# Kernel optimization log

Measured on AMD Instinct MI355X. Metric: run time of the kernel, lower is better.

## Reference

```python
import jax, jax.numpy as jnp
import numpy as np

D_MODEL = 1024
SEL_DIM = 64
CONFIGS = [(4, 32), (8, 64), (16, 128)]  # (heads, dim)
B, T = 2, 2048


def setup_inputs() -> dict:
    key = jax.random.key(0)
    ks = jax.random.split(key, 20)
    s = 0.02  # init scale for stability
    inp = {
        "x": jax.random.normal(ks[0], (B, T, D_MODEL), jnp.float32),
        "sel_w1": jax.random.normal(ks[1], (SEL_DIM, D_MODEL), jnp.float32) * s,
        "sel_b1": jnp.zeros((SEL_DIM,), jnp.float32),
        "sel_w2": jax.random.normal(ks[2], (SEL_DIM, SEL_DIM), jnp.float32) * s,
        "sel_b2": jnp.zeros((SEL_DIM,), jnp.float32),
        "sel_w3": jax.random.normal(ks[3], (len(CONFIGS), SEL_DIM), jnp.float32) * s,
        "sel_b3": jnp.zeros((len(CONFIGS),), jnp.float32),
    }
    for i, (h, d) in enumerate(CONFIGS):
        inp[f"qw{i}"] = jax.random.normal(ks[4 + 3 * i], (h * d, D_MODEL), jnp.float32) * s
        inp[f"kw{i}"] = jax.random.normal(ks[5 + 3 * i], (d, D_MODEL), jnp.float32) * s
        inp[f"ww{i}"] = jax.random.normal(ks[6 + 3 * i], (h, D_MODEL), jnp.float32) * s
    return inp


def _seq_features(x):
    # x: [b,t,d]
    b, t, d = x.shape
    seq_mean = jnp.mean(x, axis=1, keepdims=True)            # [b,1,d]
    seq_std = jnp.std(x, axis=1, keepdims=True, ddof=1)      # torch.std is unbiased
    pos = (jnp.arange(t, dtype=x.dtype) / t)[None, :, None]  # [1,t,1] broadcast to [b,t,d]
    return x + seq_mean + seq_std + pos * 0.1


def _forward(x, sel_w1, sel_b1, sel_w2, sel_b2, sel_w3, sel_b3,
             qw0, kw0, ww0, qw1, kw1, ww1, qw2, kw2, ww2):
    b, t, dm = x.shape
    feats = _seq_features(x)
    h1 = jax.nn.relu(feats @ sel_w1.T + sel_b1)
    h2 = jax.nn.relu(h1 @ sel_w2.T + sel_b2)
    config_probs = jax.nn.softmax(h2 @ sel_w3.T + sel_b3, axis=-1)  # [b,t,ncfg]

    per_cfg = [(qw0, kw0, ww0), (qw1, kw1, ww1), (qw2, kw2, ww2)]
    final = jnp.zeros((b, t, t), dtype=x.dtype)
    for i, ((heads, dim), (qw, kw, ww)) in enumerate(zip(CONFIGS, per_cfg)):
        q = (x @ qw.T).reshape(b, t, heads, dim)   # [b,t,h,d]
        k = x @ kw.T                               # [b,s,d]
        w = x @ ww.T                               # [b,t,h]
        dots = jnp.einsum('bthd,bsd->bths', q, k)  # [b,t,h,s]
        score = jnp.einsum('bths,bth->bts', jax.nn.relu(dots), w)  # relu*weight, sum heads
        final = final + config_probs[:, :, i:i + 1] * score
    return final


def reference(x, sel_w1, sel_b1, sel_w2, sel_b2, sel_w3, sel_b3,
              qw0, kw0, ww0, qw1, kw1, ww1, qw2, kw2, ww2):
    return _forward(x, sel_w1, sel_b1, sel_w2, sel_b2, sel_w3, sel_b3,
                    qw0, kw0, ww0, qw1, kw1, ww1, qw2, kw2, ww2)
```

## Files before the change

### kernel.cpp

```cpp
#include <hip/hip_runtime.h>
#include <hip/hip_fp16.h>
#include <cstdint>
#include <cstddef>
#include <math.h>

#define B_ 2
#define T_ 2048
#define D_ 1024
#define M_ (B_*T_)

#define QO0 0
#define KO0 128
#define WO0 160
#define QO1 168
#define KO1 680
#define WO1 744
#define QO2 752
#define KO2 2800
#define WO2 2928
#define SELO 2944
#define LDN 3072

typedef float f32x16 __attribute__((ext_vector_type(16)));
typedef short bf16x8 __attribute__((ext_vector_type(8)));
typedef unsigned short u16;

__device__ __forceinline__ u16 f2bf(float f) {
    unsigned int u = __float_as_uint(f);
    unsigned int r = (u + 0x7fffu + ((u >> 16) & 1u)) >> 16;
    return (u16)r;
}
__device__ __forceinline__ float bf2f(u16 b) {
    return __uint_as_float(((unsigned int)b) << 16);
}

__device__ __forceinline__ void gload16(const void* g, void* l) {
    __builtin_amdgcn_global_load_lds(
        (const __attribute__((address_space(1))) unsigned int*)g,
        (__attribute__((address_space(3))) unsigned int*)l,
        16, 0, 0);
}

__device__ __forceinline__ void stage_plane(const u16* src_base, int row_stride, int k0,
                                            int rg, int lane, u16* dst) {
    int rl  = lane >> 2;
    int row = rg * 16 + rl;
    int q   = (lane & 3) ^ (rl & 3) ^ ((rl >> 2) & 3);
    const u16* s = src_base + (size_t)row * row_stride + k0 + q * 8;
    gload16(s, dst + rg * 512);
}

__global__ void stats1(const float* __restrict__ x, float* __restrict__ part,
                       float* __restrict__ part2, u16* __restrict__ Xh) {
    int d  = blockIdx.x * 256 + threadIdx.x;
    int tc = blockIdx.y;
    int b  = blockIdx.z;
    size_t base = (size_t)b * T_ * D_ + (size_t)tc * 128 * D_ + d;
    float s = 0.f, s2 = 0.f;
    for (int t = 0; t < 128; ++t) {
        float v = x[base + (size_t)t * D_];
        s += v; s2 += v * v;
        Xh[base + (size_t)t * D_] = f2bf(v);
    }
    part [(b * 16 + tc) * D_ + d] = s;
    part2[(b * 16 + tc) * D_ + d] = s2;
}

__global__ void stats2(const float* __restrict__ part, const float* __restrict__ part2,
                       const float* __restrict__ w1,
                       float* __restrict__ msd, float* __restrict__ s1) {
    __shared__ float msL[1024];
    __shared__ float ps[64][17];
    __shared__ float pw[64][17];
    int b = blockIdx.x, tid = threadIdx.x;
    float s = 0.f, s2 = 0.f;
    for (int i = 0; i < 16; ++i) {
        s  += part [(b * 16 + i) * D_ + tid];
        s2 += part2[(b * 16 + i) * D_ + tid];
    }
    float mean = s / (float)T_;
    float var  = (s2 - (float)T_ * mean * mean) / (float)(T_ - 1);
    msL[tid] = mean + sqrtf(fmaxf(var, 0.f));
    __syncthreads();
    int j = tid >> 4, cc = tid & 15;
    float am = 0.f, aw = 0.f;
    const float* wr = w1 + (size_t)j * D_ + cc * 64;
    const float* mr = msL + cc * 64;
    for (int dd = 0; dd < 64; ++dd) { float w = wr[dd]; am += mr[dd] * w; aw += w; }
    ps[j][cc] = am; pw[j][cc] = aw;
    __syncthreads();
    if (tid < 64) {
        float sm = 0.f, sw = 0.f;
        for (int i = 0; i < 16; ++i) { sm += ps[tid][i]; sw += pw[tid][i]; }
        msd[b * 64 + tid] = sm;
        if (b == 0) s1[tid] = sw;
    }
}

__global__ void split_w(const float* __restrict__ qw0, const float* __restrict__ kw0,
                        const float* __restrict__ ww0, const float* __restrict__ qw1,
                        const float* __restrict__ kw1, const float* __restrict__ ww1,
                        const float* __restrict__ qw2, const float* __restrict__ kw2,
                        const float* __restrict__ ww2, const float* __restrict__ w1s,
                        u16* __restrict__ Wh) {
    int row = blockIdx.x;
    int col = threadIdx.x * 4;
    const float* src = nullptr;
    if      (row < 128)  src = qw0 + (size_t)row * D_;
    else if (row < 160)  src = kw0 + (size_t)(row - 128) * D_;
    else if (row < 164)  src = ww0 + (size_t)(row - 160) * D_;
    else if (row < 168)  src = nullptr;
    else if (row < 680)  src = qw1 + (size_t)(row - 168) * D_;
    else if (row < 744)  src = kw1 + (size_t)(row - 680) * D_;
    else if (row < 752)  src = ww1 + (size_t)(row - 744) * D_;
    else if (row < 2800) src = qw2 + (size_t)(row - 752) * D_;
    else if (row < 2928) src = kw2 + (size_t)(row - 2800) * D_;
    else if (row < 2944) src = ww2 + (size_t)(row - 2928) * D_;
    else if (row < 3008) src = w1s + (size_t)(row - 2944) * D_;
    float4 v = src ? *(const float4*)(src + col) : make_float4(0.f, 0.f, 0.f, 0.f);
    ushort4 h;
    h.x = f2bf(v.x); h.y = f2bf(v.y); h.z = f2bf(v.z); h.w = f2bf(v.w);
    *(ushort4*)&Wh[(size_t)row * D_ + col] = h;
}

__global__ __launch_bounds__(256, 4) void proj_gemm(
    const u16* __restrict__ Xh, const u16* __restrict__ Wh, u16* __restrict__ Ph) {
    __shared__ u16 As[2][4096], Bs[2][4096];
    int tid = threadIdx.x;
    int wave = tid >> 6, lane = tid & 63;
    int bm = blockIdx.x * 128, bn = blockIdx.y * 128;
    int wt = wave >> 1, wn = wave & 1;
    int fm = lane & 31, hv = lane >> 5;
    int tkey = (fm & 3) ^ ((fm >> 2) & 3);
    f32x16 acc[2][2];
#pragma unroll
    for (int i = 0; i < 2; ++i)
#pragma unroll
        for (int j = 0; j < 2; ++j)
#pragma unroll
            for (int r = 0; r < 16; ++r) acc[i][j][r] = 0.f;

    const u16* xh = Xh + (size_t)bm * D_;
    const u16* wh = Wh + (size_t)bn * D_;

    auto stage = [&](int buf, int k0) {
#pragma unroll
        for (int i = 0; i < 4; ++i) {
            int j = wave * 4 + i;
            int pl = j >> 3, rg = j & 7;
            stage_plane(pl ? wh : xh, D_, k0, rg, lane, pl ? Bs[buf] : As[buf]);
        }
    };

    stage(0, 0);
    for (int kc = 0; kc < 32; ++kc) {
        __syncthreads();
        if (kc + 1 < 32) stage((kc + 1) & 1, (kc + 1) * 32);
        const u16* ah = As[kc & 1];
        const u16* bh = Bs[kc & 1];
#pragma unroll
        for (int ks = 0; ks < 2; ++ks) {
            int slot8 = ((ks * 2 + hv) ^ tkey) * 8;
            bf16x8 a_h[2], b_h[2];
#pragma unroll
            for (int t = 0; t < 2; ++t) {
                a_h[t] = *(const bf16x8*)&ah[(wt * 64 + t * 32 + fm) * 32 + slot8];
                b_h[t] = *(const bf16x8*)&bh[(wn * 64 + t * 32 + fm) * 32 + slot8];
            }
#pragma unroll
            for (int ti = 0; ti < 2; ++ti)
#pragma unroll
                for (int tj = 0; tj < 2; ++tj)
                    acc[ti][tj] = __builtin_amdgcn_mfma_f32_32x32x16_bf16(a_h[ti], b_h[tj], acc[ti][tj], 0, 0, 0);
        }
    }
#pragma unroll
    for (int ti = 0; ti < 2; ++ti)
#pragma unroll
        for (int tj = 0; tj < 2; ++tj)
#pragma unroll
            for (int r = 0; r < 16; ++r) {
                int row = bm + wt * 64 + ti * 32 + (r & 3) + 8 * (r >> 2) + 4 * (lane >> 5);
                int col = bn + wn * 64 + tj * 32 + (lane & 31);
                Ph[(size_t)row * LDN + col] = f2bf(acc[ti][tj][r]);
            }
}

__global__ void selector2(const u16* __restrict__ Ph,
                          const float* __restrict__ msd, const float* __restrict__ s1,
                          const float* __restrict__ b1, const float* __restrict__ w2,
                          const float* __restrict__ b2, const float* __restrict__ w3,
                          const float* __restrict__ b3, __half* __restrict__ WP) {
    __shared__ float h1s[4][64];
    __shared__ float h2s[4][64];
    __shared__ float lg[4][3];
    int tid = threadIdx.x;
    int slot = tid >> 6, j = tid & 63;
    int bt = blockIdx.x * 4 + slot;
    int b = bt >> 11, t = bt & 2047;
    size_t pidx = (size_t)bt * LDN + SELO + j;
    float v = bf2f(Ph[pidx])
            + msd[b * 64 + j] + 0.1f * ((float)t / (float)T_) * s1[j] + b1[j];
    h1s[slot][j] = fmaxf(v, 0.f);
    __syncthreads();
    float a2 = b2[j];
#pragma unroll 8
    for (int d = 0; d < 64; ++d) a2 = fmaf(h1s[slot][d], w2[j * 64 + d], a2);
    h2s[slot][j] = fmaxf(a2, 0.f);
    __syncthreads();
    if (j < 3) {
        float a3 = b3[j];
        for (int d = 0; d < 64; ++d) a3 = fmaf(h2s[slot][d], w3[j * 64 + d], a3);
        lg[slot][j] = a3;
    }
    __syncthreads();
    if (j < 28) {
        float m = fmaxf(lg[slot][0], fmaxf(lg[slot][1], lg[slot][2]));
        float e0 = expf(lg[slot][0] - m), e1 = expf(lg[slot][1] - m), e2 = expf(lg[slot][2] - m);
        float inv = 1.f / (e0 + e1 + e2);
        int wcol = (j < 4) ? (WO0 + j) : ((j < 12) ? (WO1 + j - 4) : (WO2 + j - 12));
        float p = ((j < 4) ? e0 : ((j < 12) ? e1 : e2)) * inv;
        float w = bf2f(Ph[(size_t)bt * LDN + wcol]);
        WP[(size_t)(b * 28 + j) * T_ + t] = __float2half(w * p);
    }
}

__global__ __launch_bounds__(256, 4) void score_kernel(
    const u16* __restrict__ Ph, const __half* __restrict__ WP, float* __restrict__ out) {
    __shared__ u16 Qs[2][4096];
    __shared__ u16 Ks[4][2048];
    __shared__ __half wpL[3584];
    int tid = threadIdx.x;
    int wave = tid >> 6, lane = tid & 63;
    int wt = wave >> 1, wn = wave & 1;
    int fm = lane & 31, hv = lane >> 5;
    int tkey = (fm & 3) ^ ((fm >> 2) & 3);

    int n = blockIdx.x;
    int qt = (n & 7) * 4 + (n >> 8);
    int b = qt >> 4, t0 = (qt & 15) * 128;
    int s0 = ((n >> 3) & 31) * 64;

    const u16* Pq = Ph + (size_t)(b * T_ + t0) * LDN;
    const u16* Pk = Ph + (size_t)(b * T_ + s0) * LDN;

    auto stageQ = [&](int buf, int qcol) {
#pragma unroll
        for (int i = 0; i < 2; ++i) {
            int rg = wave * 2 + i;
            stage_plane(Pq, LDN, qcol, rg, lane, Qs[buf]);
        }
    };

#pragma unroll
    for (int i = 0; i < 3; ++i) {
        int j = i * 4 + wave;
        int pl = j >> 2, rg = j & 3;
        int col = (pl == 0) ? KO0 : ((pl == 1) ? KO1 : KO1 + 32);
        stage_plane(Pk, LDN, col, rg, lane, Ks[pl]);
    }
#pragma unroll
    for (int i = 0; i < 2; ++i) {
        int j = i * 4 + wave;
        if (j < 7) {
            const __half* src = WP + (size_t)(b * 28 + j * 4 + (lane >> 4)) * T_ + t0 + (lane & 15) * 8;
            gload16(src, (u16*)wpL + j * 512);
        }
    }
    stageQ(0, QO0);

    f32x16 outacc[2], dots[2];
#pragma unroll
    for (int i = 0; i < 2; ++i)
#pragma unroll
        for (int r = 0; r < 16; ++r) { outacc[i][r] = 0.f; dots[i][r] = 0.f; }

    for (int c = 0; c < 84; ++c) {
        int kp, g;
        if (c < 4)       { kp = 0; g = c; }
        else if (c < 20) { int u = c - 4;  kp = 1 + (u & 1); g = (u & 1) ? (4 + (u >> 1)) : -1; }
        else             { int u = c - 20; kp = u & 3; g = ((u & 3) == 3) ? (12 + (u >> 2)) : -1; }

        __syncthreads();
        if (c < 83) {
            int nc = c + 1;
            int nq = (nc < 4) ? (QO0 + nc * 32)
                   : ((nc < 20) ? (QO1 + (nc - 4) * 32) : (QO2 + (nc - 20) * 32));
            stageQ((nc) & 1, nq);
        }

        const u16* qb = Qs[c & 1];
        const u16* kb = Ks[kp];
#pragma unroll
        for (int ks = 0; ks < 2; ++ks) {
            int slot8 = ((ks * 2 + hv) ^ tkey) * 8;
            bf16x8 kf = *(const bf16x8*)&kb[(wn * 32 + fm) * 32 + slot8];
#pragma unroll
            for (int ti = 0; ti < 2; ++ti) {
                bf16x8 qf = *(const bf16x8*)&qb[(wt * 64 + ti * 32 + fm) * 32 + slot8];
                dots[ti] = __builtin_amdgcn_mfma_f32_32x32x16_bf16(qf, kf, dots[ti], 0, 0, 0);
            }
        }

        if (g >= 0) {
#pragma unroll
            for (int ti = 0; ti < 2; ++ti) {
                int rowbase = wt * 64 + ti * 32 + 4 * hv;
#pragma unroll
                for (int rq = 0; rq < 4; ++rq) {
                    const __half2* wp2 = (const __half2*)&wpL[g * 128 + rowbase + rq * 8];
                    float2 f01 = __half22float2(wp2[0]);
                    float2 f23 = __half22float2(wp2[1]);
                    float wv[4] = {f01.x, f01.y, f23.x, f23.y};
#pragma unroll
                    for (int r2 = 0; r2 < 4; ++r2) {
                        int r = rq * 4 + r2;
                        outacc[ti][r] += fmaxf(dots[ti][r], 0.f) * wv[r2];
                        dots[ti][r] = 0.f;
                    }
                }
            }
        }

        if (c == 19) {
            __syncthreads();
#pragma unroll
            for (int i = 0; i < 4; ++i) {
                int j = i * 4 + wave;
                int pl = j >> 2, rg = j & 3;
                stage_plane(Pk, LDN, KO2 + pl * 32, rg, lane, Ks[pl]);
            }
        }
    }

#pragma unroll
    for (int ti = 0; ti < 2; ++ti)
#pragma unroll
        for (int r = 0; r < 16; ++r) {
            int row = wt * 64 + ti * 32 + (r & 3) + 8 * (r >> 2) + 4 * hv;
            out[(size_t)(b * T_ + t0 + row) * T_ + s0 + wn * 32 + fm] = outacc[ti][r];
        }
}

extern "C" void kernel_launch(void* const* d_in, const int* in_sizes, int n_in,
                              void* d_out, int out_size, void* d_ws, size_t ws_size,
                              hipStream_t stream) {
    const float* x   = (const float*)d_in[0];
    const float* w1  = (const float*)d_in[1];
    const float* b1  = (const float*)d_in[2];
    const float* w2  = (const float*)d_in[3];
    const float* b2  = (const float*)d_in[4];
    const float* w3  = (const float*)d_in[5];
    const float* b3  = (const float*)d_in[6];
    const float* qw0 = (const float*)d_in[7];
    const float* kw0 = (const float*)d_in[8];
    const float* ww0 = (const float*)d_in[9];
    const float* qw1 = (const float*)d_in[10];
    const float* kw1 = (const float*)d_in[11];
    const float* ww1 = (const float*)d_in[12];
    const float* qw2 = (const float*)d_in[13];
    const float* kw2 = (const float*)d_in[14];
    const float* ww2 = (const float*)d_in[15];
    float* out = (float*)d_out;

    float* fb = (float*)d_ws;
    float* PA  = fb; fb += (size_t)B_ * 16 * D_;
    float* PA2 = fb; fb += (size_t)B_ * 16 * D_;
    float* MSD = fb; fb += 128;
    float* S1  = fb; fb += 64;
    __half* WP = (__half*)fb; fb += (size_t)B_ * 28 * T_ / 2;
    u16* ub = (u16*)fb;
    u16* Wh = ub; ub += (size_t)LDN * D_;
    u16* Xh = ub; ub += (size_t)M_ * D_;
    u16* Ph = ub; ub += (size_t)M_ * LDN;

    stats1<<<dim3(D_ / 256, 16, B_), 256, 0, stream>>>(x, PA, PA2, Xh);
    stats2<<<dim3(B_), 1024, 0, stream>>>(PA, PA2, w1, MSD, S1);
    split_w<<<dim3(LDN), 256, 0, stream>>>(qw0, kw0, ww0, qw1, kw1, ww1,
                                           qw2, kw2, ww2, w1, Wh);
    proj_gemm<<<dim3(M_ / 128, LDN / 128), 256, 0, stream>>>(Xh, Wh, Ph);
    selector2<<<dim3(M_ / 4), 256, 0, stream>>>(Ph, MSD, S1, b1, w2, b2, w3, b3, WP);
    score_kernel<<<dim3(1024), 256, 0, stream>>>(Ph, WP, out);
}
```

Baseline: 269.3 us.

## Enlarge score tiles to 128x128, widen GEMM K-chunk, split stats reduction finer

The score kernel now computes 128x128 output tiles with 64-wide head-dim phases instead of 128x64 tiles with 32-wide chunks. This halves the block count and doubles reuse of the staged Q tile, at the cost of more LDS and registers (launch bounds drop to 2). The projection GEMM switches from double-buffered 32-wide K steps to single-buffered 64-wide K steps with two barriers per step. The stats kernel splits the time axis into 128 chunks for more parallelism, which makes stats2 reduce over more partial sums.

```diff
diff --git a/kernel.cpp b/kernel.cpp
--- a/kernel.cpp
+++ b/kernel.cpp
@@ -55,15 +55,16 @@
     int d  = blockIdx.x * 256 + threadIdx.x;
     int tc = blockIdx.y;
     int b  = blockIdx.z;
-    size_t base = (size_t)b * T_ * D_ + (size_t)tc * 128 * D_ + d;
+    size_t base = (size_t)b * T_ * D_ + (size_t)tc * 16 * D_ + d;
     float s = 0.f, s2 = 0.f;
-    for (int t = 0; t < 128; ++t) {
+#pragma unroll
+    for (int t = 0; t < 16; ++t) {
         float v = x[base + (size_t)t * D_];
         s += v; s2 += v * v;
         Xh[base + (size_t)t * D_] = f2bf(v);
     }
-    part [(b * 16 + tc) * D_ + d] = s;
-    part2[(b * 16 + tc) * D_ + d] = s2;
+    part [(b * 128 + tc) * D_ + d] = s;
+    part2[(b * 128 + tc) * D_ + d] = s2;
 }
 
 __global__ void stats2(const float* __restrict__ part, const float* __restrict__ part2,
@@ -74,9 +75,10 @@
     __shared__ float pw[64][17];
     int b = blockIdx.x, tid = threadIdx.x;
     float s = 0.f, s2 = 0.f;
-    for (int i = 0; i < 16; ++i) {
-        s  += part [(b * 16 + i) * D_ + tid];
-        s2 += part2[(b * 16 + i) * D_ + tid];
+#pragma unroll 8
+    for (int i = 0; i < 128; ++i) {
+        s  += part [(b * 128 + i) * D_ + tid];
+        s2 += part2[(b * 128 + i) * D_ + tid];
     }
     float mean = s / (float)T_;
     float var  = (s2 - (float)T_ * mean * mean) / (float)(T_ - 1);
@@ -123,9 +125,9 @@
     *(ushort4*)&Wh[(size_t)row * D_ + col] = h;
 }
 
-__global__ __launch_bounds__(256, 4) void proj_gemm(
+__global__ __launch_bounds__(256, 3) void proj_gemm(
     const u16* __restrict__ Xh, const u16* __restrict__ Wh, u16* __restrict__ Ph) {
-    __shared__ u16 As[2][4096], Bs[2][4096];
+    __shared__ u16 As[8192], Bs[8192];
     int tid = threadIdx.x;
     int wave = tid >> 6, lane = tid & 63;
     int bm = blockIdx.x * 128, bn = blockIdx.y * 128;
@@ -143,29 +145,27 @@
     const u16* xh = Xh + (size_t)bm * D_;
     const u16* wh = Wh + (size_t)bn * D_;
 
-    auto stage = [&](int buf, int k0) {
-#pragma unroll
-        for (int i = 0; i < 4; ++i) {
-            int j = wave * 4 + i;
-            int pl = j >> 3, rg = j & 7;
-            stage_plane(pl ? wh : xh, D_, k0, rg, lane, pl ? Bs[buf] : As[buf]);
-        }
-    };
-
-    stage(0, 0);
-    for (int kc = 0; kc < 32; ++kc) {
-        __syncthreads();
-        if (kc + 1 < 32) stage((kc + 1) & 1, (kc + 1) * 32);
-        const u16* ah = As[kc & 1];
-        const u16* bh = Bs[kc & 1];
-#pragma unroll
-        for (int ks = 0; ks < 2; ++ks) {
-            int slot8 = ((ks * 2 + hv) ^ tkey) * 8;
+    for (int kc = 0; kc < 16; ++kc) {
+        int k0 = kc * 64;
+#pragma unroll
+        for (int i = 0; i < 8; ++i) {
+            int j = wave * 8 + i;
+            int mat = j >> 4;
+            int pl  = (j >> 3) & 1;
+            int rg  = j & 7;
+            stage_plane(mat ? wh : xh, D_, k0 + pl * 32, rg, lane,
+                        (mat ? Bs : As) + pl * 4096);
+        }
+        __syncthreads();
+#pragma unroll
+        for (int ks = 0; ks < 4; ++ks) {
+            int pl = ks >> 1;
+            int slot8 = (((ks & 1) * 2 + hv) ^ tkey) * 8;
             bf16x8 a_h[2], b_h[2];
 #pragma unroll
             for (int t = 0; t < 2; ++t) {
-                a_h[t] = *(const bf16x8*)&ah[(wt * 64 + t * 32 + fm) * 32 + slot8];
-                b_h[t] = *(const bf16x8*)&bh[(wn * 64 + t * 32 + fm) * 32 + slot8];
+                a_h[t] = *(const bf16x8*)&As[pl * 4096 + (wt * 64 + t * 32 + fm) * 32 + slot8];
+                b_h[t] = *(const bf16x8*)&Bs[pl * 4096 + (wn * 64 + t * 32 + fm) * 32 + slot8];
             }
 #pragma unroll
             for (int ti = 0; ti < 2; ++ti)
@@ -173,6 +173,7 @@
                 for (int tj = 0; tj < 2; ++tj)
                     acc[ti][tj] = __builtin_amdgcn_mfma_f32_32x32x16_bf16(a_h[ti], b_h[tj], acc[ti][tj], 0, 0, 0);
         }
+        __syncthreads();
     }
 #pragma unroll
     for (int ti = 0; ti < 2; ++ti)
@@ -180,8 +181,8 @@
         for (int tj = 0; tj < 2; ++tj)
 #pragma unroll
             for (int r = 0; r < 16; ++r) {
-                int row = bm + wt * 64 + ti * 32 + (r & 3) + 8 * (r >> 2) + 4 * (lane >> 5);
-                int col = bn + wn * 64 + tj * 32 + (lane & 31);
+                int row = bm + wt * 64 + ti * 32 + (r & 3) + 8 * (r >> 2) + 4 * hv;
+                int col = bn + wn * 64 + tj * 32 + fm;
                 Ph[(size_t)row * LDN + col] = f2bf(acc[ti][tj][r]);
             }
 }
@@ -225,10 +226,16 @@
     }
 }
 
-__global__ __launch_bounds__(256, 4) void score_kernel(
+__device__ __forceinline__ int qcol_of(int c) {
+    if (c < 2)  return QO0 + c * 64;
+    if (c < 10) return QO1 + (c - 2) * 64;
+    return QO2 + (c - 10) * 64;
+}
+
+__global__ __launch_bounds__(256, 2) void score_kernel(
     const u16* __restrict__ Ph, const __half* __restrict__ WP, float* __restrict__ out) {
-    __shared__ u16 Qs[2][4096];
-    __shared__ u16 Ks[4][2048];
+    __shared__ u16 Qs[2][8192];
+    __shared__ u16 Ks[4 * 4096];
     __shared__ __half wpL[3584];
     int tid = threadIdx.x;
     int wave = tid >> 6, lane = tid & 63;
@@ -236,28 +243,30 @@
     int fm = lane & 31, hv = lane >> 5;
     int tkey = (fm & 3) ^ ((fm >> 2) & 3);
 
-    int n = blockIdx.x;
-    int qt = (n & 7) * 4 + (n >> 8);
-    int b = qt >> 4, t0 = (qt & 15) * 128;
-    int s0 = ((n >> 3) & 31) * 64;
+    int n = blockIdx.z * 256 + blockIdx.y * 16 + blockIdx.x;
+    int p = (n & 7) * 4 + (n >> 7);
+    int xb = (n >> 3) & 15;
+    int b = p >> 4, yb = p & 15;
+    int t0 = yb * 128, s0 = xb * 128;
 
     const u16* Pq = Ph + (size_t)(b * T_ + t0) * LDN;
     const u16* Pk = Ph + (size_t)(b * T_ + s0) * LDN;
 
     auto stageQ = [&](int buf, int qcol) {
 #pragma unroll
-        for (int i = 0; i < 2; ++i) {
-            int rg = wave * 2 + i;
-            stage_plane(Pq, LDN, qcol, rg, lane, Qs[buf]);
+        for (int i = 0; i < 4; ++i) {
+            int j = (wave << 2) + i;
+            int pl = j >> 3, rg = j & 7;
+            stage_plane(Pq, LDN, qcol + pl * 32, rg, lane, &Qs[buf][pl * 4096]);
         }
     };
 
 #pragma unroll
-    for (int i = 0; i < 3; ++i) {
+    for (int i = 0; i < 6; ++i) {
         int j = i * 4 + wave;
-        int pl = j >> 2, rg = j & 3;
+        int pl = j >> 3, rg = j & 7;
         int col = (pl == 0) ? KO0 : ((pl == 1) ? KO1 : KO1 + 32);
-        stage_plane(Pk, LDN, col, rg, lane, Ks[pl]);
+        stage_plane(Pk, LDN, col, rg, lane, &Ks[pl * 4096]);
     }
 #pragma unroll
     for (int i = 0; i < 2; ++i) {
@@ -269,77 +278,101 @@
     }
     stageQ(0, QO0);
 
-    f32x16 outacc[2], dots[2];
+    f32x16 outacc[2][2], dots[2][2], Z16;
+#pragma unroll
+    for (int r = 0; r < 16; ++r) Z16[r] = 0.f;
 #pragma unroll
     for (int i = 0; i < 2; ++i)
 #pragma unroll
-        for (int r = 0; r < 16; ++r) { outacc[i][r] = 0.f; dots[i][r] = 0.f; }
-
-    for (int c = 0; c < 84; ++c) {
-        int kp, g;
-        if (c < 4)       { kp = 0; g = c; }
-        else if (c < 20) { int u = c - 4;  kp = 1 + (u & 1); g = (u & 1) ? (4 + (u >> 1)) : -1; }
-        else             { int u = c - 20; kp = u & 3; g = ((u & 3) == 3) ? (12 + (u >> 2)) : -1; }
-
-        __syncthreads();
-        if (c < 83) {
-            int nc = c + 1;
-            int nq = (nc < 4) ? (QO0 + nc * 32)
-                   : ((nc < 20) ? (QO1 + (nc - 4) * 32) : (QO2 + (nc - 20) * 32));
-            stageQ((nc) & 1, nq);
-        }
-
-        const u16* qb = Qs[c & 1];
-        const u16* kb = Ks[kp];
-#pragma unroll
-        for (int ks = 0; ks < 2; ++ks) {
-            int slot8 = ((ks * 2 + hv) ^ tkey) * 8;
-            bf16x8 kf = *(const bf16x8*)&kb[(wn * 32 + fm) * 32 + slot8];
-#pragma unroll
-            for (int ti = 0; ti < 2; ++ti) {
-                bf16x8 qf = *(const bf16x8*)&qb[(wt * 64 + ti * 32 + fm) * 32 + slot8];
-                dots[ti] = __builtin_amdgcn_mfma_f32_32x32x16_bf16(qf, kf, dots[ti], 0, 0, 0);
-            }
-        }
-
-        if (g >= 0) {
-#pragma unroll
-            for (int ti = 0; ti < 2; ++ti) {
-                int rowbase = wt * 64 + ti * 32 + 4 * hv;
-#pragma unroll
-                for (int rq = 0; rq < 4; ++rq) {
-                    const __half2* wp2 = (const __half2*)&wpL[g * 128 + rowbase + rq * 8];
-                    float2 f01 = __half22float2(wp2[0]);
-                    float2 f23 = __half22float2(wp2[1]);
-                    float wv[4] = {f01.x, f01.y, f23.x, f23.y};
+        for (int j = 0; j < 2; ++j)
+#pragma unroll
+            for (int r = 0; r < 16; ++r) { outacc[i][j][r] = 0.f; dots[i][j][r] = 0.f; }
+
+    auto epi = [&](int g) {
+#pragma unroll
+        for (int ti = 0; ti < 2; ++ti) {
+            int rowbase = wt * 64 + ti * 32 + 4 * hv;
+#pragma unroll
+            for (int rq = 0; rq < 4; ++rq) {
+                const __half2* wp2 = (const __half2*)&wpL[g * 128 + rowbase + rq * 8];
+                float2 f01 = __half22float2(wp2[0]);
+                float2 f23 = __half22float2(wp2[1]);
+                float wv[4] = {f01.x, f01.y, f23.x, f23.y};
+#pragma unroll
+                for (int tj = 0; tj < 2; ++tj)
 #pragma unroll
                     for (int r2 = 0; r2 < 4; ++r2) {
                         int r = rq * 4 + r2;
-                        outacc[ti][r] += fmaxf(dots[ti][r], 0.f) * wv[r2];
-                        dots[ti][r] = 0.f;
+                        outacc[ti][tj][r] += fmaxf(dots[ti][tj][r], 0.f) * wv[r2];
                     }
-                }
             }
         }
-
-        if (c == 19) {
+    };
+
+    auto phase64 = [&](const u16* qb, int kpA, int kpB, bool z0, bool midBreak,
+                       int gMid, bool hasEnd, int gEnd) {
+#pragma unroll
+        for (int ks = 0; ks < 4; ++ks) {
+            int kp = (ks < 2) ? kpA : kpB;
+            int slot8 = (((ks & 1) * 2 + hv) ^ tkey) * 8;
+            bool zero = (ks == 0 && z0) || (ks == 2 && midBreak);
+            bf16x8 kf[2], qf[2];
+#pragma unroll
+            for (int tj = 0; tj < 2; ++tj)
+                kf[tj] = *(const bf16x8*)&Ks[kp * 4096 + (wn * 64 + tj * 32 + fm) * 32 + slot8];
+#pragma unroll
+            for (int ti = 0; ti < 2; ++ti)
+                qf[ti] = *(const bf16x8*)&qb[(ks >> 1) * 4096 + (wt * 64 + ti * 32 + fm) * 32 + slot8];
+#pragma unroll
+            for (int ti = 0; ti < 2; ++ti)
+#pragma unroll
+                for (int tj = 0; tj < 2; ++tj)
+                    dots[ti][tj] = __builtin_amdgcn_mfma_f32_32x32x16_bf16(
+                        qf[ti], kf[tj], zero ? Z16 : dots[ti][tj], 0, 0, 0);
+            if (ks == 1 && midBreak) epi(gMid);
+            if (ks == 3 && hasEnd)   epi(gEnd);
+        }
+    };
+
+#pragma unroll
+    for (int c = 0; c < 2; ++c) {
+        __syncthreads();
+        stageQ((c + 1) & 1, qcol_of(c + 1));
+        phase64(Qs[c & 1], 0, 0, true, true, 2 * c, true, 2 * c + 1);
+    }
+    for (int h = 0; h < 8; ++h) {
+        int c = 2 + h;
+        __syncthreads();
+        stageQ((c + 1) & 1, qcol_of(c + 1));
+        phase64(Qs[c & 1], 1, 2, true, false, -1, true, 4 + h);
+        if (h == 7) {
             __syncthreads();
-#pragma unroll
-            for (int i = 0; i < 4; ++i) {
-                int j = i * 4 + wave;
-                int pl = j >> 2, rg = j & 3;
-                stage_plane(Pk, LDN, KO2 + pl * 32, rg, lane, Ks[pl]);
+            for (int j = wave; j < 32; j += 4) {
+                int pl = j >> 3, rg = j & 7;
+                stage_plane(Pk, LDN, KO2 + pl * 32, rg, lane, &Ks[pl * 4096]);
             }
         }
     }
+    for (int h = 0; h < 16; ++h) {
+        int c = 10 + 2 * h;
+        __syncthreads();
+        stageQ((c + 1) & 1, qcol_of(c + 1));
+        phase64(Qs[c & 1], 0, 1, true, false, -1, false, -1);
+        __syncthreads();
+        if (c + 1 < 41) stageQ(c & 1, qcol_of(c + 2));
+        phase64(Qs[(c + 1) & 1], 2, 3, false, false, -1, true, 12 + h);
+    }
 
 #pragma unroll
     for (int ti = 0; ti < 2; ++ti)
 #pragma unroll
-        for (int r = 0; r < 16; ++r) {
-            int row = wt * 64 + ti * 32 + (r & 3) + 8 * (r >> 2) + 4 * hv;
-            out[(size_t)(b * T_ + t0 + row) * T_ + s0 + wn * 32 + fm] = outacc[ti][r];
-        }
+        for (int tj = 0; tj < 2; ++tj)
+#pragma unroll
+            for (int r = 0; r < 16; ++r) {
+                int trow = wt * 64 + ti * 32 + (r & 3) + 8 * (r >> 2) + 4 * hv;
+                int scol = wn * 64 + tj * 32 + fm;
+                out[(size_t)(b * T_ + t0 + trow) * T_ + (s0 + scol)] = outacc[ti][tj][r];
+            }
 }
 
 extern "C" void kernel_launch(void* const* d_in, const int* in_sizes, int n_in,
@@ -364,8 +397,8 @@
     float* out = (float*)d_out;
 
     float* fb = (float*)d_ws;
-    float* PA  = fb; fb += (size_t)B_ * 16 * D_;
-    float* PA2 = fb; fb += (size_t)B_ * 16 * D_;
+    float* PA  = fb; fb += (size_t)B_ * 128 * D_;
+    float* PA2 = fb; fb += (size_t)B_ * 128 * D_;
     float* MSD = fb; fb += 128;
     float* S1  = fb; fb += 64;
     __half* WP = (__half*)fb; fb += (size_t)B_ * 28 * T_ / 2;
@@ -374,11 +407,11 @@
     u16* Xh = ub; ub += (size_t)M_ * D_;
     u16* Ph = ub; ub += (size_t)M_ * LDN;
 
-    stats1<<<dim3(D_ / 256, 16, B_), 256, 0, stream>>>(x, PA, PA2, Xh);
+    stats1<<<dim3(D_ / 256, 128, B_), 256, 0, stream>>>(x, PA, PA2, Xh);
     stats2<<<dim3(B_), 1024, 0, stream>>>(PA, PA2, w1, MSD, S1);
     split_w<<<dim3(LDN), 256, 0, stream>>>(qw0, kw0, ww0, qw1, kw1, ww1,
                                            qw2, kw2, ww2, w1, Wh);
     proj_gemm<<<dim3(M_ / 128, LDN / 128), 256, 0, stream>>>(Xh, Wh, Ph);
     selector2<<<dim3(M_ / 4), 256, 0, stream>>>(Ph, MSD, S1, b1, w2, b2, w3, b3, WP);
-    score_kernel<<<dim3(1024), 256, 0, stream>>>(Ph, WP, out);
-}
+    score_kernel<<<dim3(T_ / 128, T_ / 128, B_), 256, 0, stream>>>(Ph, WP, out);
+}
```

Result: faster. 256.8 us (-4.7%).
